# Performance work log

Measured on AMD Instinct MI355X. Metric: run time of the kernel, lower is better.

Reference implementation:

```python
import jax, jax.numpy as jnp
import numpy as np

MAX_LEVEL = 50

def _ln(x, g, b, eps=1e-5):
    m = jnp.mean(x, axis=-1, keepdims=True)
    v = jnp.mean((x - m) ** 2, axis=-1, keepdims=True)
    return (x - m) * jax.lax.rsqrt(v + eps) * g + b

def _mlp2(x, w1, b1, w2, b2):
    return jax.nn.relu(x @ w1 + b1) @ w2 + b2

def _forward(tokens, ln_g, ln_b, pw1, pb1, pw2, pb2, emb,
             sw1, sb1, sw2, sb2, ew1, eb1, ew2, eb2,
             spw1, spb1, spw2, spb2, lw1, lb1, lw2, lb2,
             fw, fb, fg, fbeta, aW, ab, ag, abt,
             dw1, db1, dw2, db2, levels, ph, pw):
    N = tokens.shape[0]
    f32 = tokens.dtype
    # token_norm + token_projection (Dropout is identity in eval)
    x = _ln(tokens, ln_g, ln_b)
    h = jax.nn.gelu(x @ pw1 + pb1, approximate=False) @ pw2 + pb2  # [N, D]
    idx = jnp.clip(levels[:, 0], 0, MAX_LEVEL)  # [N]
    h = h + emb[idx]
    # feature enhancement branch
    var = jnp.var(tokens, axis=-1, ddof=1, keepdims=True)            # torch.var unbiased
    mean = jnp.mean(tokens, axis=-1, keepdims=True)
    edge = jnp.mean(jnp.abs(jnp.diff(tokens, axis=-1)), axis=-1, keepdims=True)
    stats_feat = _mlp2(jnp.concatenate([var, mean], -1), sw1, sb1, sw2, sb2)
    spatial = jnp.broadcast_to(jnp.array([[ph, pw]], dtype=f32), (N, 2))
    spatial_feat = _mlp2(spatial, spw1, spb1, spw2, spb2)
    edge_feat = _mlp2(edge, ew1, eb1, ew2, eb2)
    lvl = jnp.broadcast_to(levels[0, 0].astype(f32)[None, None], (N, 1))
    level_feat = _mlp2(lvl, lw1, lb1, lw2, lb2)
    enh = jnp.concatenate([stats_feat, edge_feat, spatial_feat, level_feat], -1)  # [N, D]
    enh = jax.nn.gelu(_ln(enh @ fw + fb, fg, fbeta), approximate=False)
    h = h + 0.3 * enh
    # per-token scale adapter: MoE-style gather + tiny per-token GEMM + per-expert LN + GELU
    y = jnp.einsum('nd,ndf->nf', h, aW[idx]) + ab[idx]
    y = jax.nn.gelu(_ln(y, ag[idx], abt[idx]), approximate=False)
    # dynamic weighting gate
    w = jax.nn.sigmoid(_mlp2(y, dw1, db1, dw2, db2))  # [N, 1]
    return y * (0.8 + 0.4 * w)


def setup_inputs() -> dict:
    key = jax.random.key(0)
    ks = iter(jax.random.split(key, 64))
    def rn(shape, s=0.02):
        return jax.random.normal(next(ks), shape, dtype=jnp.float32) * s
    IN, D, D2, D4, DH, E, N = 768, 256, 512, 64, 128, 51, 4096
    return {
        'tokens': jax.random.normal(next(ks), (N, IN), dtype=jnp.float32),
        'ln_g': jnp.ones((IN,)), 'ln_b': jnp.zeros((IN,)),
        'pw1': rn((IN, D2)), 'pb1': jnp.zeros((D2,)),
        'pw2': rn((D2, D)), 'pb2': jnp.zeros((D,)),
        'emb': rn((E, D), 1.0),
        'sw1': rn((2, D4)), 'sb1': jnp.zeros((D4,)), 'sw2': rn((D4, D4)), 'sb2': jnp.zeros((D4,)),
        'ew1': rn((1, D4)), 'eb1': jnp.zeros((D4,)), 'ew2': rn((D4, D4)), 'eb2': jnp.zeros((D4,)),
        'spw1': rn((2, D4)), 'spb1': jnp.zeros((D4,)), 'spw2': rn((D4, D4)), 'spb2': jnp.zeros((D4,)),
        'lw1': rn((1, D4)), 'lb1': jnp.zeros((D4,)), 'lw2': rn((D4, D4)), 'lb2': jnp.zeros((D4,)),
        'fw': rn((D, D)), 'fb': jnp.zeros((D,)), 'fg': jnp.ones((D,)), 'fbeta': jnp.zeros((D,)),
        'aW': rn((E, D, D)), 'ab': jnp.zeros((E, D)), 'ag': jnp.ones((E, D)), 'abt': jnp.zeros((E, D)),
        'dw1': rn((D, DH)), 'db1': jnp.zeros((DH,)), 'dw2': rn((DH, 1)), 'db2': jnp.zeros((1,)),
        'levels': jax.random.randint(next(ks), (N, 2), 0, E),
        'ph': 4, 'pw': 4,
    }


def reference(tokens, ln_g, ln_b, pw1, pb1, pw2, pb2, emb,
              sw1, sb1, sw2, sb2, ew1, eb1, ew2, eb2,
              spw1, spb1, spw2, spb2, lw1, lb1, lw2, lb2,
              fw, fb, fg, fbeta, aW, ab, ag, abt,
              dw1, db1, dw2, db2, levels, ph, pw):
    return _forward(tokens, ln_g, ln_b, pw1, pb1, pw2, pb2, emb,
                    sw1, sb1, sw2, sb2, ew1, eb1, ew2, eb2,
                    spw1, spb1, spw2, spb2, lw1, lb1, lw2, lb2,
                    fw, fb, fg, fbeta, aW, ab, ag, abt,
                    dw1, db1, dw2, db2, levels, ph, pw)
```

## Files before the change

### kernel.cpp

```cpp
#include <hip/hip_runtime.h>
#include <math.h>

#define NTOK 4096
#define IND 768
#define DD 256
#define DD2 512
#define DHH 128
#define NEXP 51
#define TM 16
#define NTILE_MAX 312
#define NWCONV 968

typedef __attribute__((ext_vector_type(4))) float f32x4;
typedef __attribute__((ext_vector_type(8))) short short8;

__device__ __forceinline__ float gelu_f(float x) {
    return 0.5f * x * (1.0f + erff(x * 0.70710678118654752440f));
}
__device__ __forceinline__ ushort f2bf(float x) {
    unsigned u = __float_as_uint(x);
    return (ushort)((u + 0x7fffu + ((u >> 16) & 1u)) >> 16);
}
__device__ __forceinline__ void gl_lds16(const ushort* g, ushort* l) {
    __builtin_amdgcn_global_load_lds(
        (const __attribute__((address_space(1))) unsigned int*)g,
        (__attribute__((address_space(3))) unsigned int*)l, 16, 0, 0);
}

__global__ __launch_bounds__(256) void k_pre(
    const float* __restrict__ pw1, const float* __restrict__ pw2,
    const float* __restrict__ fw, const float* __restrict__ dw1,
    const float* __restrict__ aW,
    ushort* __restrict__ pw1T, ushort* __restrict__ pw2T, ushort* __restrict__ fwT,
    ushort* __restrict__ dw1T, ushort* __restrict__ aWT,
    const float* __restrict__ tokens,
    const float* __restrict__ ln_g, const float* __restrict__ ln_b,
    const float* __restrict__ sw1, const float* __restrict__ sb1,
    const float* __restrict__ sw2, const float* __restrict__ sb2,
    const float* __restrict__ ew1, const float* __restrict__ eb1,
    const float* __restrict__ ew2, const float* __restrict__ eb2,
    ushort* __restrict__ x_ln, ushort* __restrict__ enh,
    const int* __restrict__ levels,
    const float* __restrict__ spw1, const float* __restrict__ spb1,
    const float* __restrict__ spw2, const float* __restrict__ spb2,
    const float* __restrict__ lw1, const float* __restrict__ lb1,
    const float* __restrict__ lw2, const float* __restrict__ lb2,
    const int* __restrict__ ph, const int* __restrict__ pw,
    const float* __restrict__ fb,
    int* __restrict__ sorted, int* __restrict__ tpos, int* __restrict__ tcnt,
    int* __restrict__ texp, int* __restrict__ meta, float* __restrict__ ctail) {
    __shared__ float T[64][65];
    __shared__ int cnt[NEXP], cur[NEXP], offS[NEXP + 1], tileoff[NEXP + 1];
    __shared__ int expS[NTOK];
    __shared__ float hsS[64], hlS[64], cf[128];
    int t = threadIdx.x;

    if (blockIdx.x == 0) {
        if (t < NEXP) cnt[t] = 0;
        if (t < 64) {
            float p0 = (float)ph[0], p1 = (float)pw[0];
            float lvl = (float)levels[0];
            hsS[t] = fmaxf(0.f, p0 * spw1[t] + p1 * spw1[64 + t] + spb1[t]);
            hlS[t] = fmaxf(0.f, lvl * lw1[t] + lb1[t]);
        }
        __syncthreads();
        int myidx[16];
        #pragma unroll
        for (int i = 0; i < 16; ++i) {
            int n = t + i * 256;
            int id = min(max(levels[n * 2], 0), NEXP - 1);
            myidx[i] = id;
            atomicAdd(&cnt[id], 1);
        }
        if (t < 64) {
            float v = spb2[t];
            for (int j = 0; j < 64; ++j) v += hsS[j] * spw2[j * 64 + t];
            cf[t] = v;
        } else if (t < 128) {
            int k = t - 64;
            float v = lb2[k];
            for (int j = 0; j < 64; ++j) v += hlS[j] * lw2[j * 64 + k];
            cf[64 + k] = v;
        }
        __syncthreads();
        if (t == 0) {
            int a = 0, ta = 0;
            for (int e = 0; e < NEXP; ++e) {
                offS[e] = a; cur[e] = a; tileoff[e] = ta;
                ta += (cnt[e] + TM - 1) / TM;
                a += cnt[e];
            }
            offS[NEXP] = a; tileoff[NEXP] = ta;
            meta[0] = ta;
        }
        __syncthreads();
        #pragma unroll
        for (int i = 0; i < 16; ++i) {
            int n = t + i * 256;
            int p = atomicAdd(&cur[myidx[i]], 1);
            sorted[p] = n;
            expS[p] = myidx[i];
        }
        {
            float v = fb[t];
            for (int j = 0; j < 128; ++j) v += cf[j] * fw[(size_t)(128 + j) * DD + t];
            ctail[t] = v;
        }
        __syncthreads();
        #pragma unroll
        for (int i = 0; i < 16; ++i) {
            int p = t + i * 256;
            int e = expS[p];
            int rel = p - offS[e];
            if ((rel & (TM - 1)) == 0) {
                int ti = tileoff[e] + (rel / TM);
                tpos[ti] = p;
                tcnt[ti] = min(TM, offS[e + 1] - p);
                texp[ti] = e;
            }
        }
        return;
    }
    if (blockIdx.x < 1 + NWCONV) {
        int b = blockIdx.x - 1;
        const float* src; ushort* dst; int R, C;
        if (b < 96)       { src = pw1; dst = pw1T; R = IND; C = DD2; }
        else if (b < 128) { b -= 96;  src = pw2; dst = pw2T; R = DD2; C = DD; }
        else if (b < 144) { b -= 128; src = fw;  dst = fwT;  R = DD;  C = DD; }
        else if (b < 152) { b -= 144; src = dw1; dst = dw1T; R = DD;  C = DHH; }
        else { b -= 152; int e = b >> 4; b &= 15;
               src = aW + (size_t)e * DD * DD; dst = aWT + (size_t)e * DD * DD;
               R = DD; C = DD; }
        int tpc = C >> 6;
        int tr = b / tpc, tc = b - tr * tpc;
        int lr = t >> 6, lc = t & 63;
        #pragma unroll
        for (int i = 0; i < 16; ++i) {
            int r = i * 4 + lr;
            T[r][lc] = src[(size_t)(tr * 64 + r) * C + tc * 64 + lc];
        }
        __syncthreads();
        #pragma unroll
        for (int i = 0; i < 16; ++i) {
            int r = i * 4 + lr;
            dst[(size_t)(tc * 64 + r) * R + tr * 64 + lc] = f2bf(T[lc][r]);
        }
        return;
    }
    {
        int w = t >> 6, lane = t & 63;
        int n = (blockIdx.x - 1 - NWCONV) * 4 + w;
        const float* x = tokens + (size_t)n * IND;
        float v[12];
        {
            float4 va = *(const float4*)(x + lane * 12);
            float4 vb = *(const float4*)(x + lane * 12 + 4);
            float4 vc = *(const float4*)(x + lane * 12 + 8);
            v[0]=va.x; v[1]=va.y; v[2]=va.z; v[3]=va.w;
            v[4]=vb.x; v[5]=vb.y; v[6]=vb.z; v[7]=vb.w;
            v[8]=vc.x; v[9]=vc.y; v[10]=vc.z; v[11]=vc.w;
        }
        float s = 0.f, s2 = 0.f, es = 0.f;
        #pragma unroll
        for (int j = 0; j < 12; ++j) { s += v[j]; s2 += v[j] * v[j]; }
        float prev = __shfl_up(v[11], 1);
        if (lane > 0) es += fabsf(v[0] - prev);
        #pragma unroll
        for (int j = 1; j < 12; ++j) es += fabsf(v[j] - v[j - 1]);
        #pragma unroll
        for (int o = 1; o < 64; o <<= 1) {
            s  += __shfl_xor(s, o);
            s2 += __shfl_xor(s2, o);
            es += __shfl_xor(es, o);
        }
        float mean = s * (1.f / 768.f);
        float var_u = (s2 - 768.f * mean * mean) * (1.f / 767.f);
        float rstd = rsqrtf(s2 * (1.f / 768.f) - mean * mean + 1e-5f);
        float edge = es * (1.f / 767.f);
        ushort xl[12];
        #pragma unroll
        for (int j = 0; j < 12; ++j) {
            int e = lane * 12 + j;
            xl[j] = f2bf((v[j] - mean) * rstd * ln_g[e] + ln_b[e]);
        }
        ushort* xd = x_ln + (size_t)n * IND + lane * 12;
        *(ushort4*)(xd)     = *(ushort4*)&xl[0];
        *(ushort4*)(xd + 4) = *(ushort4*)&xl[4];
        *(ushort4*)(xd + 8) = *(ushort4*)&xl[8];
        float hs_ = fmaxf(0.f, var_u * sw1[lane] + mean * sw1[64 + lane] + sb1[lane]);
        float he_ = fmaxf(0.f, edge * ew1[lane] + eb1[lane]);
        float acc_s = sb2[lane], acc_e = eb2[lane];
        #pragma unroll 8
        for (int j = 0; j < 64; ++j) {
            float hj = __shfl(hs_, j);
            float ej = __shfl(he_, j);
            acc_s += hj * sw2[j * 64 + lane];
            acc_e += ej * ew2[j * 64 + lane];
        }
        ushort* er = enh + (size_t)n * DHH;
        er[lane] = f2bf(acc_s);
        er[64 + lane] = f2bf(acc_e);
    }
}

__global__ __launch_bounds__(512) void k_gemm1(
    const ushort* __restrict__ A, const ushort* __restrict__ BT,
    const float* __restrict__ bias, ushort* __restrict__ Cb) {
    const int N = DD2, K = IND;
    __shared__ ushort Al[128][64];
    __shared__ ushort Bl[64][64];
    int tid = threadIdx.x;
    int w = tid >> 6, lane = tid & 63;
    int g = lane >> 4, mr = lane & 15;
    int mq = w >> 1, nq = w & 1;
    int bm = blockIdx.y * 128, bn = blockIdx.x * 64;
    int r8 = lane >> 3, c = lane & 7, cg = c ^ r8;
    f32x4 acc[2][2];
    #pragma unroll
    for (int im = 0; im < 2; ++im)
        #pragma unroll
        for (int in = 0; in < 2; ++in) acc[im][in] = (f32x4){0.f, 0.f, 0.f, 0.f};
    for (int k0 = 0; k0 < K; k0 += 64) {
        #pragma unroll
        for (int i = 0; i < 2; ++i) {
            int r = 16 * w + 8 * i + r8;
            gl_lds16(A + (size_t)(bm + r) * K + k0 + cg * 8, &Al[16 * w + 8 * i][0]);
        }
        {
            int r = 8 * w + r8;
            gl_lds16(BT + (size_t)(bn + r) * K + k0 + cg * 8, &Bl[8 * w][0]);
        }
        asm volatile("s_waitcnt vmcnt(0)" ::: "memory");
        __syncthreads();
        #pragma unroll
        for (int kk = 0; kk < 64; kk += 32) {
            int jc = (kk >> 3) + g;
            int sw = ((jc ^ (mr & 7)) << 4);
            #pragma unroll
            for (int im = 0; im < 2; ++im) {
                short8 av = *(const short8*)((const char*)&Al[0][0] + (32 * mq + 16 * im + mr) * 128 + sw);
                #pragma unroll
                for (int in = 0; in < 2; ++in) {
                    short8 bv = *(const short8*)((const char*)&Bl[0][0] + (32 * nq + 16 * in + mr) * 128 + sw);
                    acc[im][in] = __builtin_amdgcn_mfma_f32_16x16x32_bf16(av, bv, acc[im][in], 0, 0, 0);
                }
            }
        }
        __syncthreads();
    }
    #pragma unroll
    for (int im = 0; im < 2; ++im) {
        #pragma unroll
        for (int in = 0; in < 2; ++in) {
            int col = bn + 32 * nq + 16 * in + mr;
            float bv = bias[col];
            #pragma unroll
            for (int r = 0; r < 4; ++r) {
                int row = bm + 32 * mq + 16 * im + 4 * g + r;
                Cb[(size_t)row * N + col] = f2bf(gelu_f(acc[im][in][r] + bv));
            }
        }
    }
}

__global__ __launch_bounds__(256) void k_adapterF(
    const ushort* __restrict__ h1, const ushort* __restrict__ enh,
    const ushort* __restrict__ pw2T, const float* __restrict__ pb2,
    const float* __restrict__ emb,
    const ushort* __restrict__ fwT, const float* __restrict__ ctail,
    const float* __restrict__ fg, const float* __restrict__ fbeta,
    const ushort* __restrict__ aWT, const float* __restrict__ ab,
    const float* __restrict__ ag, const float* __restrict__ abt,
    const ushort* __restrict__ dw1T, const float* __restrict__ db1,
    const float* __restrict__ dw2, const float* __restrict__ db2,
    const int* __restrict__ sorted, const int* __restrict__ tpos,
    const int* __restrict__ tcnt, const int* __restrict__ texp,
    const int* __restrict__ meta, float* __restrict__ out) {
    __shared__ __align__(16) char smA[16384];
    __shared__ __align__(16) char smB[32768];
    __shared__ __align__(16) ushort Alf[TM][264];
    __shared__ __align__(16) ushort EnhS[TM][128];
    __shared__ int tokS[TM];
    __shared__ float redS[4][TM][2];
    __shared__ float gateS[TM];
    __shared__ float pg[4][TM];
    ushort* H1p = (ushort*)smA;
    ushort* Dlp = (ushort*)smA;
    ushort* Blp = (ushort*)smB;
    float* yf32 = (float*)smB;

    int b = blockIdx.x;
    if (b >= meta[0]) return;
    int tid = threadIdx.x, w = tid >> 6, lane = tid & 63;
    int g = lane >> 4, mr = lane & 15;
    int r8 = lane >> 3, c = lane & 7, cg = c ^ r8;
    int e = texp[b], base = tpos[b], nv = tcnt[b];
    if (tid < TM) tokS[tid] = sorted[base + min(tid, nv - 1)];
    __syncthreads();

    #pragma unroll
    for (int i = 0; i < 4; ++i) {
        int r = 4 * w + i;
        int tok = tokS[r];
        gl_lds16(h1 + (size_t)tok * DD2 + ((lane ^ (r & 7)) << 3), H1p + r * DD2);
    }
    {
        int row = 4 * w + (lane >> 4);
        int tok = tokS[row];
        int ch = lane & 15;
        gl_lds16(enh + (size_t)tok * DHH + ((ch ^ (row & 7)) << 3), &EnhS[4 * w][0]);
    }
    asm volatile("s_waitcnt vmcnt(0)" ::: "memory");
    __syncthreads();

    f32x4 hacc[4];
    #pragma unroll
    for (int q = 0; q < 4; ++q) hacc[q] = (f32x4){0.f, 0.f, 0.f, 0.f};
    for (int k0 = 0; k0 < DD2; k0 += 64) {
        #pragma unroll
        for (int i = 0; i < 8; ++i) {
            int r = 64 * w + 8 * i + r8;
            gl_lds16(pw2T + (size_t)r * DD2 + k0 + cg * 8, Blp + (64 * w + 8 * i) * 64);
        }
        asm volatile("s_waitcnt vmcnt(0)" ::: "memory");
        __syncthreads();
        #pragma unroll
        for (int kk = 0; kk < 64; kk += 32) {
            int jc = ((k0 + kk) >> 3) + g;
            short8 av = *(const short8*)((const char*)H1p + mr * 1024 + ((jc ^ (mr & 7)) << 4));
            int swb = (((kk >> 3) + g) ^ (mr & 7)) << 4;
            #pragma unroll
            for (int q = 0; q < 4; ++q) {
                short8 bv = *(const short8*)((const char*)Blp + (64 * w + 16 * q + mr) * 128 + swb);
                hacc[q] = __builtin_amdgcn_mfma_f32_16x16x32_bf16(av, bv, hacc[q], 0, 0, 0);
            }
        }
        __syncthreads();
    }
    f32x4 eacc[4];
    #pragma unroll
    for (int q = 0; q < 4; ++q) eacc[q] = (f32x4){0.f, 0.f, 0.f, 0.f};
    for (int k0 = 0; k0 < DHH; k0 += 64) {
        #pragma unroll
        for (int i = 0; i < 8; ++i) {
            int r = 64 * w + 8 * i + r8;
            gl_lds16(fwT + (size_t)r * DD + k0 + cg * 8, Blp + (64 * w + 8 * i) * 64);
        }
        asm volatile("s_waitcnt vmcnt(0)" ::: "memory");
        __syncthreads();
        #pragma unroll
        for (int kk = 0; kk < 64; kk += 32) {
            int jc = ((k0 + kk) >> 3) + g;
            short8 av = *(const short8*)((const char*)&EnhS[0][0] + mr * 256 + ((jc ^ (mr & 7)) << 4));
            int swb = (((kk >> 3) + g) ^ (mr & 7)) << 4;
            #pragma unroll
            for (int q = 0; q < 4; ++q) {
                short8 bv = *(const short8*)((const char*)Blp + (64 * w + 16 * q + mr) * 128 + swb);
                eacc[q] = __builtin_amdgcn_mfma_f32_16x16x32_bf16(av, bv, eacc[q], 0, 0, 0);
            }
        }
        __syncthreads();
    }
    #pragma unroll
    for (int q = 0; q < 4; ++q) {
        int col = 64 * w + 16 * q + mr;
        float hb = pb2[col] + emb[(size_t)e * DD + col];
        float cb2 = ctail[col];
        #pragma unroll
        for (int r4 = 0; r4 < 4; ++r4) {
            hacc[q][r4] += hb;
            eacc[q][r4] += cb2;
        }
    }
    {
        float s[4], s2[4];
        #pragma unroll
        for (int r4 = 0; r4 < 4; ++r4) {
            s[r4] = eacc[0][r4] + eacc[1][r4] + eacc[2][r4] + eacc[3][r4];
            s2[r4] = eacc[0][r4]*eacc[0][r4] + eacc[1][r4]*eacc[1][r4]
                   + eacc[2][r4]*eacc[2][r4] + eacc[3][r4]*eacc[3][r4];
        }
        #pragma unroll
        for (int o = 1; o < 16; o <<= 1) {
            #pragma unroll
            for (int r4 = 0; r4 < 4; ++r4) {
                s[r4]  += __shfl_xor(s[r4], o);
                s2[r4] += __shfl_xor(s2[r4], o);
            }
        }
        if (mr == 0) {
            #pragma unroll
            for (int r4 = 0; r4 < 4; ++r4) {
                redS[w][4 * g + r4][0] = s[r4];
                redS[w][4 * g + r4][1] = s2[r4];
            }
        }
    }
    __syncthreads();
    #pragma unroll
    for (int r4 = 0; r4 < 4; ++r4) {
        int row = 4 * g + r4;
        float S  = redS[0][row][0] + redS[1][row][0] + redS[2][row][0] + redS[3][row][0];
        float S2 = redS[0][row][1] + redS[1][row][1] + redS[2][row][1] + redS[3][row][1];
        float m = S * (1.f / 256.f);
        float rs = rsqrtf(S2 * (1.f / 256.f) - m * m + 1e-5f);
        #pragma unroll
        for (int q = 0; q < 4; ++q) {
            int col = 64 * w + 16 * q + mr;
            float enhv = gelu_f((eacc[q][r4] - m) * rs * fg[col] + fbeta[col]);
            Alf[row][col] = f2bf(hacc[q][r4] + 0.3f * enhv);
        }
    }
    __syncthreads();
    const ushort* We = aWT + (size_t)e * DD * DD;
    f32x4 yacc[4];
    #pragma unroll
    for (int q = 0; q < 4; ++q) yacc[q] = (f32x4){0.f, 0.f, 0.f, 0.f};
    for (int k0 = 0; k0 < DD; k0 += 64) {
        #pragma unroll
        for (int i = 0; i < 8; ++i) {
            int r = 64 * w + 8 * i + r8;
            gl_lds16(We + (size_t)r * DD + k0 + cg * 8, Blp + (64 * w + 8 * i) * 64);
        }
        asm volatile("s_waitcnt vmcnt(0)" ::: "memory");
        __syncthreads();
        #pragma unroll
        for (int kk = 0; kk < 64; kk += 32) {
            short8 av = *(const short8*)&Alf[mr][k0 + kk + g * 8];
            int swb = (((kk >> 3) + g) ^ (mr & 7)) << 4;
            #pragma unroll
            for (int q = 0; q < 4; ++q) {
                short8 bv = *(const short8*)((const char*)Blp + (64 * w + 16 * q + mr) * 128 + swb);
                yacc[q] = __builtin_amdgcn_mfma_f32_16x16x32_bf16(av, bv, yacc[q], 0, 0, 0);
            }
        }
        __syncthreads();
    }
    #pragma unroll
    for (int q = 0; q < 4; ++q) {
        int col = 64 * w + 16 * q + mr;
        float abv = ab[(size_t)e * DD + col];
        #pragma unroll
        for (int r4 = 0; r4 < 4; ++r4) {
            yf32[(4 * g + r4) * 260 + col] = yacc[q][r4] + abv;
        }
    }
    __syncthreads();
    #pragma unroll
    for (int i = 0; i < 4; ++i) {
        int r = w * 4 + i;
        float4 v = *(const float4*)&yf32[r * 260 + lane * 4];
        float s = v.x + v.y + v.z + v.w;
        float s2 = v.x * v.x + v.y * v.y + v.z * v.z + v.w * v.w;
        #pragma unroll
        for (int o = 1; o < 64; o <<= 1) { s += __shfl_xor(s, o); s2 += __shfl_xor(s2, o); }
        float m = s * (1.f / 256.f);
        float rs = rsqrtf(s2 * (1.f / 256.f) - m * m + 1e-5f);
        float4 gg = *(const float4*)(ag + (size_t)e * DD + lane * 4);
        float4 bb = *(const float4*)(abt + (size_t)e * DD + lane * 4);
        float4 y;
        y.x = gelu_f((v.x - m) * rs * gg.x + bb.x);
        y.y = gelu_f((v.y - m) * rs * gg.y + bb.y);
        y.z = gelu_f((v.z - m) * rs * gg.z + bb.z);
        y.w = gelu_f((v.w - m) * rs * gg.w + bb.w);
        *(float4*)&yf32[r * 260 + lane * 4] = y;
        ushort4 o4 = {f2bf(y.x), f2bf(y.y), f2bf(y.z), f2bf(y.w)};
        *(ushort4*)&Alf[r][lane * 4] = o4;
    }
    __syncthreads();
    f32x4 acc2[2];
    acc2[0] = (f32x4){0.f, 0.f, 0.f, 0.f};
    acc2[1] = (f32x4){0.f, 0.f, 0.f, 0.f};
    for (int k0 = 0; k0 < DD; k0 += 64) {
        #pragma unroll
        for (int i = 0; i < 4; ++i) {
            int r = 32 * w + 8 * i + r8;
            gl_lds16(dw1T + (size_t)r * DD + k0 + cg * 8, Dlp + (32 * w + 8 * i) * 64);
        }
        asm volatile("s_waitcnt vmcnt(0)" ::: "memory");
        __syncthreads();
        #pragma unroll
        for (int kk = 0; kk < 64; kk += 32) {
            short8 av = *(const short8*)&Alf[mr][k0 + kk + g * 8];
            int swb = (((kk >> 3) + g) ^ (mr & 7)) << 4;
            #pragma unroll
            for (int q = 0; q < 2; ++q) {
                short8 bv = *(const short8*)((const char*)Dlp + (32 * w + 16 * q + mr) * 128 + swb);
                acc2[q] = __builtin_amdgcn_mfma_f32_16x16x32_bf16(av, bv, acc2[q], 0, 0, 0);
            }
        }
        __syncthreads();
    }
    float pv[4] = {0.f, 0.f, 0.f, 0.f};
    #pragma unroll
    for (int q = 0; q < 2; ++q) {
        int col = 32 * w + 16 * q + mr;
        float d1 = db1[col], d2 = dw2[col];
        #pragma unroll
        for (int r4 = 0; r4 < 4; ++r4)
            pv[r4] += fmaxf(acc2[q][r4] + d1, 0.f) * d2;
    }
    #pragma unroll
    for (int o = 1; o < 16; o <<= 1) {
        #pragma unroll
        for (int r4 = 0; r4 < 4; ++r4) pv[r4] += __shfl_xor(pv[r4], o);
    }
    if (mr == 0) {
        #pragma unroll
        for (int r4 = 0; r4 < 4; ++r4)
            pg[w][4 * g + r4] = pv[r4];
    }
    __syncthreads();
    if (tid < TM) {
        float p = pg[0][tid] + pg[1][tid] + pg[2][tid] + pg[3][tid] + db2[0];
        gateS[tid] = 0.8f + 0.4f / (1.f + expf(-p));
    }
    __syncthreads();
    {
        int row = tid >> 4, c0 = (tid & 15) * 16;
        if (row < nv) {
            int tok = tokS[row];
            float gt = gateS[row];
            #pragma unroll
            for (int j = 0; j < 4; ++j) {
                float4 v = *(const float4*)&yf32[row * 260 + c0 + j * 4];
                v.x *= gt; v.y *= gt; v.z *= gt; v.w *= gt;
                *(float4*)(out + (size_t)tok * DD + c0 + j * 4) = v;
            }
        }
    }
}

extern "C" void kernel_launch(void* const* d_in, const int* in_sizes, int n_in,
                              void* d_out, int out_size, void* d_ws, size_t ws_size,
                              hipStream_t stream) {
    const float* tokens = (const float*)d_in[0];
    const float* ln_g = (const float*)d_in[1];
    const float* ln_b = (const float*)d_in[2];
    const float* pw1 = (const float*)d_in[3];
    const float* pb1 = (const float*)d_in[4];
    const float* pw2 = (const float*)d_in[5];
    const float* pb2 = (const float*)d_in[6];
    const float* emb = (const float*)d_in[7];
    const float* sw1 = (const float*)d_in[8];
    const float* sb1 = (const float*)d_in[9];
    const float* sw2 = (const float*)d_in[10];
    const float* sb2 = (const float*)d_in[11];
    const float* ew1 = (const float*)d_in[12];
    const float* eb1 = (const float*)d_in[13];
    const float* ew2 = (const float*)d_in[14];
    const float* eb2 = (const float*)d_in[15];
    const float* spw1 = (const float*)d_in[16];
    const float* spb1 = (const float*)d_in[17];
    const float* spw2 = (const float*)d_in[18];
    const float* spb2 = (const float*)d_in[19];
    const float* lw1 = (const float*)d_in[20];
    const float* lb1 = (const float*)d_in[21];
    const float* lw2 = (const float*)d_in[22];
    const float* lb2 = (const float*)d_in[23];
    const float* fw = (const float*)d_in[24];
    const float* fb = (const float*)d_in[25];
    const float* fg = (const float*)d_in[26];
    const float* fbeta = (const float*)d_in[27];
    const float* aW = (const float*)d_in[28];
    const float* ab = (const float*)d_in[29];
    const float* ag = (const float*)d_in[30];
    const float* abt = (const float*)d_in[31];
    const float* dw1 = (const float*)d_in[32];
    const float* db1 = (const float*)d_in[33];
    const float* dw2 = (const float*)d_in[34];
    const float* db2 = (const float*)d_in[35];
    const int* levels = (const int*)d_in[36];
    const int* ph = (const int*)d_in[37];
    const int* pw = (const int*)d_in[38];
    float* outp = (float*)d_out;

    char* wsb = (char*)d_ws;
    ushort* x_ln  = (ushort*)wsb;  wsb += (size_t)NTOK * IND * 2;
    ushort* h1    = (ushort*)wsb;  wsb += (size_t)NTOK * DD2 * 2;
    ushort* enh   = (ushort*)wsb;  wsb += (size_t)NTOK * DHH * 2;
    ushort* pw1T  = (ushort*)wsb;  wsb += (size_t)DD2 * IND * 2;
    ushort* pw2T  = (ushort*)wsb;  wsb += (size_t)DD * DD2 * 2;
    ushort* fwT   = (ushort*)wsb;  wsb += (size_t)DD * DD * 2;
    ushort* aWT   = (ushort*)wsb;  wsb += (size_t)NEXP * DD * DD * 2;
    ushort* dw1T  = (ushort*)wsb;  wsb += (size_t)DHH * DD * 2;
    float*  ctail = (float*)wsb;   wsb += DD * 4;
    int*    sorted = (int*)wsb;    wsb += NTOK * 4;
    int*    tpos   = (int*)wsb;    wsb += NTILE_MAX * 4;
    int*    tcnt   = (int*)wsb;    wsb += NTILE_MAX * 4;
    int*    texp   = (int*)wsb;    wsb += NTILE_MAX * 4;
    int*    meta   = (int*)wsb;    wsb += 64;

    k_pre<<<1 + NWCONV + NTOK / 4, 256, 0, stream>>>(
        pw1, pw2, fw, dw1, aW, pw1T, pw2T, fwT, dw1T, aWT,
        tokens, ln_g, ln_b, sw1, sb1, sw2, sb2, ew1, eb1, ew2, eb2,
        x_ln, enh, levels,
        spw1, spb1, spw2, spb2, lw1, lb1, lw2, lb2, ph, pw, fb,
        sorted, tpos, tcnt, texp, meta, ctail);
    k_gemm1<<<dim3(DD2 / 64, NTOK / 128), 512, 0, stream>>>(x_ln, pw1T, pb1, h1);
    k_adapterF<<<NTILE_MAX, 256, 0, stream>>>(
        h1, enh, pw2T, pb2, emb, fwT, ctail, fg, fbeta,
        aWT, ab, ag, abt, dw1T, db1, dw2, db2,
        sorted, tpos, tcnt, texp, meta, outp);
}
```

Before: 64.51 us.

## Double adapter tile to 32 tokens with 512 threads per block

Raises the per-expert token tile in the fused adapter kernel from 16 to 32 rows and runs 8 waves per block, two waves per 64-column slice covering the two 16-row halves. Each block now loads the pw2, fw, per-expert aW and dw1 weight tiles once for twice as many tokens, which halves weight traffic per token and cuts the tile count. Shared memory is reorganised so the activation buffer aliases the h1 staging area. In exchange, more tiles are partially filled for experts with few tokens, and the larger shared-memory footprint per block lowers occupancy.

```diff
diff --git a/kernel.cpp b/kernel.cpp
--- a/kernel.cpp
+++ b/kernel.cpp
@@ -7,8 +7,8 @@
 #define DD2 512
 #define DHH 128
 #define NEXP 51
-#define TM 16
-#define NTILE_MAX 312
+#define TM 32
+#define NTILE_MAX 179
 #define NWCONV 968
 
 typedef __attribute__((ext_vector_type(4))) float f32x4;
@@ -263,7 +263,7 @@
     }
 }
 
-__global__ __launch_bounds__(256) void k_adapterF(
+__global__ __launch_bounds__(512) void k_adapterF(
     const ushort* __restrict__ h1, const ushort* __restrict__ enh,
     const ushort* __restrict__ pw2T, const float* __restrict__ pb2,
     const float* __restrict__ emb,
@@ -276,16 +276,16 @@
     const int* __restrict__ sorted, const int* __restrict__ tpos,
     const int* __restrict__ tcnt, const int* __restrict__ texp,
     const int* __restrict__ meta, float* __restrict__ out) {
-    __shared__ __align__(16) char smA[16384];
-    __shared__ __align__(16) char smB[32768];
-    __shared__ __align__(16) ushort Alf[TM][264];
+    __shared__ __align__(16) char smA[33280];
+    __shared__ __align__(16) char smB[33280];
     __shared__ __align__(16) ushort EnhS[TM][128];
     __shared__ int tokS[TM];
     __shared__ float redS[4][TM][2];
     __shared__ float gateS[TM];
     __shared__ float pg[4][TM];
     ushort* H1p = (ushort*)smA;
-    ushort* Dlp = (ushort*)smA;
+    ushort* Alf = (ushort*)smA;
+    ushort* Dlp = (ushort*)(smA + 16896);
     ushort* Blp = (ushort*)smB;
     float* yf32 = (float*)smB;
 
@@ -294,6 +294,7 @@
     int tid = threadIdx.x, w = tid >> 6, lane = tid & 63;
     int g = lane >> 4, mr = lane & 15;
     int r8 = lane >> 3, c = lane & 7, cg = c ^ r8;
+    int mt = w & 1, cb = 64 * (w >> 1);
     int e = texp[b], base = tpos[b], nv = tcnt[b];
     if (tid < TM) tokS[tid] = sorted[base + min(tid, nv - 1)];
     __syncthreads();
@@ -318,20 +319,20 @@
     for (int q = 0; q < 4; ++q) hacc[q] = (f32x4){0.f, 0.f, 0.f, 0.f};
     for (int k0 = 0; k0 < DD2; k0 += 64) {
         #pragma unroll
-        for (int i = 0; i < 8; ++i) {
-            int r = 64 * w + 8 * i + r8;
-            gl_lds16(pw2T + (size_t)r * DD2 + k0 + cg * 8, Blp + (64 * w + 8 * i) * 64);
+        for (int i = 0; i < 4; ++i) {
+            int r = 32 * w + 8 * i + r8;
+            gl_lds16(pw2T + (size_t)r * DD2 + k0 + cg * 8, Blp + (32 * w + 8 * i) * 64);
         }
         asm volatile("s_waitcnt vmcnt(0)" ::: "memory");
         __syncthreads();
         #pragma unroll
         for (int kk = 0; kk < 64; kk += 32) {
             int jc = ((k0 + kk) >> 3) + g;
-            short8 av = *(const short8*)((const char*)H1p + mr * 1024 + ((jc ^ (mr & 7)) << 4));
+            short8 av = *(const short8*)((const char*)H1p + (16 * mt + mr) * 1024 + ((jc ^ (mr & 7)) << 4));
             int swb = (((kk >> 3) + g) ^ (mr & 7)) << 4;
             #pragma unroll
             for (int q = 0; q < 4; ++q) {
-                short8 bv = *(const short8*)((const char*)Blp + (64 * w + 16 * q + mr) * 128 + swb);
+                short8 bv = *(const short8*)((const char*)Blp + (cb + 16 * q + mr) * 128 + swb);
                 hacc[q] = __builtin_amdgcn_mfma_f32_16x16x32_bf16(av, bv, hacc[q], 0, 0, 0);
             }
         }
@@ -342,20 +343,20 @@
     for (int q = 0; q < 4; ++q) eacc[q] = (f32x4){0.f, 0.f, 0.f, 0.f};
     for (int k0 = 0; k0 < DHH; k0 += 64) {
         #pragma unroll
-        for (int i = 0; i < 8; ++i) {
-            int r = 64 * w + 8 * i + r8;
-            gl_lds16(fwT + (size_t)r * DD + k0 + cg * 8, Blp + (64 * w + 8 * i) * 64);
+        for (int i = 0; i < 4; ++i) {
+            int r = 32 * w + 8 * i + r8;
+            gl_lds16(fwT + (size_t)r * DD + k0 + cg * 8, Blp + (32 * w + 8 * i) * 64);
         }
         asm volatile("s_waitcnt vmcnt(0)" ::: "memory");
         __syncthreads();
         #pragma unroll
         for (int kk = 0; kk < 64; kk += 32) {
             int jc = ((k0 + kk) >> 3) + g;
-            short8 av = *(const short8*)((const char*)&EnhS[0][0] + mr * 256 + ((jc ^ (mr & 7)) << 4));
+            short8 av = *(const short8*)((const char*)&EnhS[0][0] + (16 * mt + mr) * 256 + ((jc ^ (mr & 7)) << 4));
             int swb = (((kk >> 3) + g) ^ (mr & 7)) << 4;
             #pragma unroll
             for (int q = 0; q < 4; ++q) {
-                short8 bv = *(const short8*)((const char*)Blp + (64 * w + 16 * q + mr) * 128 + swb);
+                short8 bv = *(const short8*)((const char*)Blp + (cb + 16 * q + mr) * 128 + swb);
                 eacc[q] = __builtin_amdgcn_mfma_f32_16x16x32_bf16(av, bv, eacc[q], 0, 0, 0);
             }
         }
@@ -363,7 +364,7 @@
     }
     #pragma unroll
     for (int q = 0; q < 4; ++q) {
-        int col = 64 * w + 16 * q + mr;
+        int col = cb + 16 * q + mr;
         float hb = pb2[col] + emb[(size_t)e * DD + col];
         float cb2 = ctail[col];
         #pragma unroll
@@ -391,24 +392,25 @@
         if (mr == 0) {
             #pragma unroll
             for (int r4 = 0; r4 < 4; ++r4) {
-                redS[w][4 * g + r4][0] = s[r4];
-                redS[w][4 * g + r4][1] = s2[r4];
+                int row = 16 * mt + 4 * g + r4;
+                redS[w >> 1][row][0] = s[r4];
+                redS[w >> 1][row][1] = s2[r4];
             }
         }
     }
     __syncthreads();
     #pragma unroll
     for (int r4 = 0; r4 < 4; ++r4) {
-        int row = 4 * g + r4;
+        int row = 16 * mt + 4 * g + r4;
         float S  = redS[0][row][0] + redS[1][row][0] + redS[2][row][0] + redS[3][row][0];
         float S2 = redS[0][row][1] + redS[1][row][1] + redS[2][row][1] + redS[3][row][1];
         float m = S * (1.f / 256.f);
         float rs = rsqrtf(S2 * (1.f / 256.f) - m * m + 1e-5f);
         #pragma unroll
         for (int q = 0; q < 4; ++q) {
-            int col = 64 * w + 16 * q + mr;
+            int col = cb + 16 * q + mr;
             float enhv = gelu_f((eacc[q][r4] - m) * rs * fg[col] + fbeta[col]);
-            Alf[row][col] = f2bf(hacc[q][r4] + 0.3f * enhv);
+            Alf[row * 264 + col] = f2bf(hacc[q][r4] + 0.3f * enhv);
         }
     }
     __syncthreads();
@@ -418,19 +420,19 @@
     for (int q = 0; q < 4; ++q) yacc[q] = (f32x4){0.f, 0.f, 0.f, 0.f};
     for (int k0 = 0; k0 < DD; k0 += 64) {
         #pragma unroll
-        for (int i = 0; i < 8; ++i) {
-            int r = 64 * w + 8 * i + r8;
-            gl_lds16(We + (size_t)r * DD + k0 + cg * 8, Blp + (64 * w + 8 * i) * 64);
+        for (int i = 0; i < 4; ++i) {
+            int r = 32 * w + 8 * i + r8;
+            gl_lds16(We + (size_t)r * DD + k0 + cg * 8, Blp + (32 * w + 8 * i) * 64);
         }
         asm volatile("s_waitcnt vmcnt(0)" ::: "memory");
         __syncthreads();
         #pragma unroll
         for (int kk = 0; kk < 64; kk += 32) {
-            short8 av = *(const short8*)&Alf[mr][k0 + kk + g * 8];
+            short8 av = *(const short8*)&Alf[(16 * mt + mr) * 264 + k0 + kk + g * 8];
             int swb = (((kk >> 3) + g) ^ (mr & 7)) << 4;
             #pragma unroll
             for (int q = 0; q < 4; ++q) {
-                short8 bv = *(const short8*)((const char*)Blp + (64 * w + 16 * q + mr) * 128 + swb);
+                short8 bv = *(const short8*)((const char*)Blp + (cb + 16 * q + mr) * 128 + swb);
                 yacc[q] = __builtin_amdgcn_mfma_f32_16x16x32_bf16(av, bv, yacc[q], 0, 0, 0);
             }
         }
@@ -438,17 +440,18 @@
     }
     #pragma unroll
     for (int q = 0; q < 4; ++q) {
-        int col = 64 * w + 16 * q + mr;
+        int col = cb + 16 * q + mr;
         float abv = ab[(size_t)e * DD + col];
         #pragma unroll
         for (int r4 = 0; r4 < 4; ++r4) {
-            yf32[(4 * g + r4) * 260 + col] = yacc[q][r4] + abv;
+            int row = 16 * mt + 4 * g + r4;
+            yf32[row * 260 + col] = yacc[q][r4] + abv;
         }
     }
     __syncthreads();
     #pragma unroll
     for (int i = 0; i < 4; ++i) {
-        int r = w * 4 + i;
+        int r = 4 * w + i;
         float4 v = *(const float4*)&yf32[r * 260 + lane * 4];
         float s = v.x + v.y + v.z + v.w;
         float s2 = v.x * v.x + v.y * v.y + v.z * v.z + v.w * v.w;
@@ -465,7 +468,7 @@
         y.w = gelu_f((v.w - m) * rs * gg.w + bb.w);
         *(float4*)&yf32[r * 260 + lane * 4] = y;
         ushort4 o4 = {f2bf(y.x), f2bf(y.y), f2bf(y.z), f2bf(y.w)};
-        *(ushort4*)&Alf[r][lane * 4] = o4;
+        *(ushort4*)&Alf[r * 264 + lane * 4] = o4;
     }
     __syncthreads();
     f32x4 acc2[2];
@@ -473,19 +476,19 @@
     acc2[1] = (f32x4){0.f, 0.f, 0.f, 0.f};
     for (int k0 = 0; k0 < DD; k0 += 64) {
         #pragma unroll
-        for (int i = 0; i < 4; ++i) {
-            int r = 32 * w + 8 * i + r8;
-            gl_lds16(dw1T + (size_t)r * DD + k0 + cg * 8, Dlp + (32 * w + 8 * i) * 64);
+        for (int i = 0; i < 2; ++i) {
+            int r = 16 * w + 8 * i + r8;
+            gl_lds16(dw1T + (size_t)r * DD + k0 + cg * 8, Dlp + (16 * w + 8 * i) * 64);
         }
         asm volatile("s_waitcnt vmcnt(0)" ::: "memory");
         __syncthreads();
         #pragma unroll
         for (int kk = 0; kk < 64; kk += 32) {
-            short8 av = *(const short8*)&Alf[mr][k0 + kk + g * 8];
+            short8 av = *(const short8*)&Alf[(16 * mt + mr) * 264 + k0 + kk + g * 8];
             int swb = (((kk >> 3) + g) ^ (mr & 7)) << 4;
             #pragma unroll
             for (int q = 0; q < 2; ++q) {
-                short8 bv = *(const short8*)((const char*)Dlp + (32 * w + 16 * q + mr) * 128 + swb);
+                short8 bv = *(const short8*)((const char*)Dlp + (32 * (w >> 1) + 16 * q + mr) * 128 + swb);
                 acc2[q] = __builtin_amdgcn_mfma_f32_16x16x32_bf16(av, bv, acc2[q], 0, 0, 0);
             }
         }
@@ -494,7 +497,7 @@
     float pv[4] = {0.f, 0.f, 0.f, 0.f};
     #pragma unroll
     for (int q = 0; q < 2; ++q) {
-        int col = 32 * w + 16 * q + mr;
+        int col = 32 * (w >> 1) + 16 * q + mr;
         float d1 = db1[col], d2 = dw2[col];
         #pragma unroll
         for (int r4 = 0; r4 < 4; ++r4)
@@ -508,7 +511,7 @@
     if (mr == 0) {
         #pragma unroll
         for (int r4 = 0; r4 < 4; ++r4)
-            pg[w][4 * g + r4] = pv[r4];
+            pg[w >> 1][16 * mt + 4 * g + r4] = pv[r4];
     }
     __syncthreads();
     if (tid < TM) {
@@ -598,7 +601,7 @@
         spw1, spb1, spw2, spb2, lw1, lb1, lw2, lb2, ph, pw, fb,
         sorted, tpos, tcnt, texp, meta, ctail);
     k_gemm1<<<dim3(DD2 / 64, NTOK / 128), 512, 0, stream>>>(x_ln, pw1T, pb1, h1);
-    k_adapterF<<<NTILE_MAX, 256, 0, stream>>>(
+    k_adapterF<<<NTILE_MAX, 512, 0, stream>>>(
         h1, enh, pw2T, pb2, emb, fwT, ctail, fg, fbeta,
         aWT, ab, ag, abt, dw1T, db1, dw2, db2,
         sorted, tpos, tcnt, texp, meta, outp);
```

Result: no change. 65.50 us (+1.5%).
